# Performance work log

Hardware: AMD Instinct MI355X
Metric: run time of the kernel (lower is better)

Reference implementation:

```python
import jax, jax.numpy as jnp
import numpy as np
from jax import lax

POOL_OUT = 20  # SOCA AdaptiveAvgPool2d((20,20))
MID = 16       # out_channel // 2
BN_EPS = 1e-3


def _pool_matrix(n, out):
    # Row-stochastic matrix replicating torch AdaptiveAvgPool2d bin boundaries:
    # start = floor(i*n/out), end = ceil((i+1)*n/out)
    P = np.zeros((out, n), np.float32)
    for i in range(out):
        s = (i * n) // out
        e = -((-(i + 1) * n) // out)
        P[i, s:e] = 1.0 / (e - s)
    return jnp.asarray(P)


def setup_inputs() -> dict:
    key = jax.random.key(0)
    ks = jax.random.split(key, 5)
    B, C, H, W = 16, 256, 128, 128
    OC = 32
    x = jax.random.normal(ks[0], (B, C, H, W), dtype=jnp.float32)
    linear_w = jax.random.normal(ks[1], (C, C), dtype=jnp.float32) * (1.0 / np.sqrt(C))
    linear_b = jnp.zeros((C,), jnp.float32)
    lsa_w = jax.random.normal(ks[2], (1, 2, 7, 7), dtype=jnp.float32) * 0.1  # Conv2d(2,1,7) no bias
    conv_w = jax.random.normal(ks[3], (OC, OC, 3, 3), dtype=jnp.float32) * (1.0 / np.sqrt(OC * 9))
    conv_b = jnp.zeros((OC,), jnp.float32)
    bn_gamma = jnp.ones((OC,), jnp.float32)
    bn_beta = jnp.zeros((OC,), jnp.float32)
    return {"x": x, "linear_w": linear_w, "linear_b": linear_b, "lsa_w": lsa_w,
            "conv_w": conv_w, "conv_b": conv_b, "bn_gamma": bn_gamma, "bn_beta": bn_beta}


def _bsa_forward(x, linear_w, linear_b, lsa_w, conv_w, conv_b, bn_gamma, bn_beta):
    b, c, h, w = x.shape
    # ---- SOCA: second-order channel attention ----
    PH = _pool_matrix(h, POOL_OUT)
    PW = _pool_matrix(w, POOL_OUT)
    xp = jnp.einsum('oh,bchw,pw->bcop', PH, x, PW)          # (b,c,20,20)
    n = POOL_OUT * POOL_OUT
    v = xp.reshape(b, c, n).transpose(0, 2, 1)               # (b,400,c)
    vc = v - v.mean(axis=1, keepdims=True)
    cov = jnp.einsum('bnc,bnd->bcd', vc, vc) / (n - 1)       # (b,c,c)
    feat = cov.mean(axis=2)                                  # (b,c)
    attn = jax.nn.sigmoid(feat @ linear_w.T + linear_b)      # (b,c)
    # ---- channel scoring / top-k selection ----
    score = attn.mean(axis=0)                                # (c,)
    score_id = jnp.argsort(-score)                           # descending
    max_id = jnp.sort(score_id[:MID])                        # (MID,)
    x1 = jnp.take(x, max_id, axis=1) * (1.0 + score[max_id])[None, :, None, None]
    # ---- grouped channel mean (c divisible by MID by construction) ----
    g = c // MID
    x2 = x.reshape(b, MID, g, h, w).mean(axis=2)             # (b,MID,h,w)
    xc = jnp.concatenate([x1, x2], axis=1)                   # (b,32,h,w)
    # ---- LSA spatial attention ----
    s = jnp.concatenate([xc.mean(axis=1, keepdims=True),
                         xc.max(axis=1, keepdims=True)], axis=1)  # (b,2,h,w)
    a = lax.conv_general_dilated(s, lsa_w, (1, 1), [(3, 3), (3, 3)],
                                 dimension_numbers=('NCHW', 'OIHW', 'NCHW'))
    xa = xc * jax.nn.sigmoid(a)
    # ---- CBA: conv(3x3, stride 2) + BN(train stats) + SiLU ----
    y = lax.conv_general_dilated(xa, conv_w, (2, 2), [(1, 1), (1, 1)],
                                 dimension_numbers=('NCHW', 'OIHW', 'NCHW'))
    y = y + conv_b[None, :, None, None]
    mu = y.mean(axis=(0, 2, 3))
    var = y.var(axis=(0, 2, 3))
    yn = (y - mu[None, :, None, None]) * lax.rsqrt(var + BN_EPS)[None, :, None, None]
    yn = yn * bn_gamma[None, :, None, None] + bn_beta[None, :, None, None]
    return yn * jax.nn.sigmoid(yn)  # SiLU


def reference(x, linear_w, linear_b, lsa_w, conv_w, conv_b, bn_gamma, bn_beta):
    return _bsa_forward(x, linear_w, linear_b, lsa_w, conv_w, conv_b, bn_gamma, bn_beta)
```

## Files before the change

kernel.cpp:

```cpp
#include <hip/hip_runtime.h>
#include <math.h>

#define B_ 16
#define C_ 256
#define H_ 128
#define W_ 128
#define HW_ (H_*W_)
#define PO 20
#define NPOOL (PO*PO)
#define MID_ 16
#define OC_ 32
#define OH_ 64
#define OW_ 64
#define BN_EPS 1e-3f

#define OFF_XP     0
#define OFF_FEAT   1638400
#define OFF_SCORE  1642496
#define OFF_MAXID  1642752
#define OFF_SCALE  1642768
#define OFF_BNSUM  1642784
#define OFF_BNSQ   1642816
#define OFF_SMEAN  1642848
#define OFF_SMAX   1904992
#define OFF_SIGA   2167136
#define OFF_XC     2429280

__device__ __forceinline__ int bin_s(int p) { return (p * 128) / 20; }
__device__ __forceinline__ int bin_e(int p) { return ((p + 1) * 128 + 19) / 20; }

__global__ __launch_bounds__(256) void k_pool2(const float* __restrict__ x,
                                               float* __restrict__ xp,
                                               float* __restrict__ xc) {
  __shared__ float tmp[64 * 21];
  const int blk = blockIdx.x;
  const int b = blk >> 5, g = (blk >> 1) & 15, rh = blk & 1;
  const int tid = threadIdx.x;
  const int hl = tid >> 2, q = tid & 3;
  const int hg = rh * 64 + hl;
  const float* rowbase = x + (size_t)(b * C_) * HW_ + (size_t)hg * W_ + q * 32;

  float4 xacc[8];
#pragma unroll
  for (int j = 0; j < 8; ++j) xacc[j] = make_float4(0.f, 0.f, 0.f, 0.f);

  for (int k = 0; k < 16; ++k) {
    const int c = g * 16 + k;
    const float4* src4 = (const float4*)(rowbase + (size_t)c * HW_);
    float bin[5];
#pragma unroll
    for (int p = 0; p < 5; ++p) bin[p] = 0.f;
#pragma unroll
    for (int j = 0; j < 8; ++j) {
      float4 v = src4[j];
      xacc[j].x += v.x; xacc[j].y += v.y; xacc[j].z += v.z; xacc[j].w += v.w;
      const float c4[4] = {v.x, v.y, v.z, v.w};
#pragma unroll
      for (int kk = 0; kk < 4; ++kk) {
        const int cc = 4 * j + kk;
#pragma unroll
        for (int p = 0; p < 5; ++p) {
          const int S = (p * 32) / 5;
          const int E = ((p + 1) * 32 + 4) / 5;
          if (cc >= S && cc < E) bin[p] += c4[kk];
        }
      }
    }
#pragma unroll
    for (int p = 0; p < 5; ++p) {
      const int S = (p * 32) / 5, E = ((p + 1) * 32 + 4) / 5;
      tmp[hl * 21 + q * 5 + p] = bin[p] / (float)(E - S);
    }
    __syncthreads();
    if (tid < 200) {
      const int ol = tid / 20, p = tid % 20;
      const int o = rh * 10 + ol;
      const int rs = bin_s(o), re = bin_e(o);
      float s = 0.f;
      for (int r = rs; r < re; ++r) s += tmp[(r - rh * 64) * 21 + p];
      xp[(size_t)(b * C_ + c) * NPOOL + o * PO + p] = s / (float)(re - rs);
    }
    __syncthreads();
  }
  float4* dst = (float4*)(xc + (size_t)(b * OC_ + MID_ + g) * HW_ + (size_t)hg * W_ + q * 32);
#pragma unroll
  for (int j = 0; j < 8; ++j) {
    float4 v = xacc[j];
    v.x *= 0.0625f; v.y *= 0.0625f; v.z *= 0.0625f; v.w *= 0.0625f;
    dst[j] = v;
  }
}

__global__ __launch_bounds__(256) void k_feat(const float* __restrict__ xp,
                                              float* __restrict__ feat) {
  const int b = blockIdx.x;
  const float* base = xp + (size_t)b * C_ * NPOOL;
  const int tid = threadIdx.x;
  __shared__ float sn[NPOOL];
  __shared__ float red[256];
  const float4* row4 = (const float4*)(base + tid * NPOOL);
  float rs = 0.f;
#pragma unroll 4
  for (int n = 0; n < NPOOL / 4; ++n) {
    float4 v = row4[n];
    rs += v.x + v.y + v.z + v.w;
  }
  float m = rs / (float)NPOOL;
  red[tid] = m;
  __syncthreads();
  for (int s = 128; s > 0; s >>= 1) {
    if (tid < s) red[tid] += red[tid + s];
    __syncthreads();
  }
  float totm = red[0];
  for (int n = tid; n < NPOOL; n += 256) {
    float cs = 0.f;
    for (int c = 0; c < C_; ++c) cs += base[c * NPOOL + n];
    sn[n] = cs - totm;
  }
  __syncthreads();
  float Sl = 0.f;
  for (int n = tid; n < NPOOL; n += 256) Sl += sn[n];
  red[tid] = Sl;
  __syncthreads();
  for (int s = 128; s > 0; s >>= 1) {
    if (tid < s) red[tid] += red[tid + s];
    __syncthreads();
  }
  float S = red[0];
  float acc = 0.f;
#pragma unroll 4
  for (int n4 = 0; n4 < NPOOL / 4; ++n4) {
    float4 v = row4[n4];
    acc += v.x * sn[4 * n4] + v.y * sn[4 * n4 + 1] + v.z * sn[4 * n4 + 2] + v.w * sn[4 * n4 + 3];
  }
  feat[b * C_ + tid] = (acc - m * S) / ((float)(NPOOL - 1) * (float)C_);
}

__global__ __launch_bounds__(256) void k_attn(const float* __restrict__ feat,
                                              const float* __restrict__ lw,
                                              const float* __restrict__ lb,
                                              float* __restrict__ score) {
  __shared__ float sf[B_ * 257];
  __shared__ float wc[16 * 257];
  __shared__ float zs[16 * 17];
  const int tid = threadIdx.x;
  const int j0 = blockIdx.x * 16;
  for (int i = tid; i < B_ * C_; i += 256) sf[(i >> 8) * 257 + (i & 255)] = feat[i];
  for (int i = tid; i < 16 * C_; i += 256)
    wc[(i >> 8) * 257 + (i & 255)] = lw[(size_t)(j0 + (i >> 8)) * C_ + (i & 255)];
  __syncthreads();
  const int jl = tid >> 4, bb = tid & 15;
  float z = 0.f;
#pragma unroll 8
  for (int i = 0; i < C_; ++i) z += sf[bb * 257 + i] * wc[jl * 257 + i];
  z += lb[j0 + jl];
  zs[jl * 17 + bb] = 1.0f / (1.0f + expf(-z));
  __syncthreads();
  if (tid < 16) {
    float s = 0.f;
#pragma unroll
    for (int k = 0; k < 16; ++k) s += zs[tid * 17 + k];
    score[j0 + tid] = s / (float)B_;
  }
}

__global__ __launch_bounds__(256) void k_select(const float* __restrict__ score,
                                                int* __restrict__ max_id,
                                                float* __restrict__ scale) {
  __shared__ float ss[C_];
  __shared__ int flag[C_];
  const int tid = threadIdx.x;
  ss[tid] = score[tid];
  __syncthreads();
  float my = ss[tid];
  int rank = 0;
  for (int k = 0; k < C_; ++k) {
    float v = ss[k];
    rank += (v > my || (v == my && k < tid)) ? 1 : 0;
  }
  flag[tid] = (rank < MID_) ? 1 : 0;
  __syncthreads();
  if (rank < MID_) {
    int pos = 0;
    for (int k = 0; k < tid; ++k) pos += flag[k];
    max_id[pos] = tid;
    scale[pos] = 1.0f + my;
  }
}

__global__ __launch_bounds__(128) void k_build(const float* __restrict__ x,
                                               const int* __restrict__ max_id,
                                               const float* __restrict__ scale,
                                               float* __restrict__ xc,
                                               float* __restrict__ smean,
                                               float* __restrict__ smax) {
  __shared__ int mid_s[MID_];
  __shared__ float sc_s[MID_];
  if (threadIdx.x < MID_) {
    mid_s[threadIdx.x] = max_id[threadIdx.x];
    sc_s[threadIdx.x] = scale[threadIdx.x];
  }
  __syncthreads();
  const int P = blockIdx.x * 128 + threadIdx.x;
  const int b = P >> 12, pix4 = P & 4095;
  const float4* xb = (const float4*)x + (size_t)(b * C_) * (HW_ / 4) + pix4;
  float4* xcb = (float4*)xc + (size_t)(b * OC_) * (HW_ / 4) + pix4;
  float4 ms = make_float4(0.f, 0.f, 0.f, 0.f);
  float4 mx = make_float4(-INFINITY, -INFINITY, -INFINITY, -INFINITY);
#pragma unroll
  for (int m = 0; m < MID_; ++m) {
    float4 t = xb[(size_t)mid_s[m] * (HW_ / 4)];
    float sc = sc_s[m];
    t.x *= sc; t.y *= sc; t.z *= sc; t.w *= sc;
    xcb[(size_t)m * (HW_ / 4)] = t;
    ms.x += t.x; ms.y += t.y; ms.z += t.z; ms.w += t.w;
    mx.x = fmaxf(mx.x, t.x); mx.y = fmaxf(mx.y, t.y);
    mx.z = fmaxf(mx.z, t.z); mx.w = fmaxf(mx.w, t.w);
  }
#pragma unroll
  for (int g = 0; g < MID_; ++g) {
    float4 t = xcb[(size_t)(MID_ + g) * (HW_ / 4)];
    ms.x += t.x; ms.y += t.y; ms.z += t.z; ms.w += t.w;
    mx.x = fmaxf(mx.x, t.x); mx.y = fmaxf(mx.y, t.y);
    mx.z = fmaxf(mx.z, t.z); mx.w = fmaxf(mx.w, t.w);
  }
  ms.x *= (1.f / 32.f); ms.y *= (1.f / 32.f); ms.z *= (1.f / 32.f); ms.w *= (1.f / 32.f);
  ((float4*)smean)[P] = ms;
  ((float4*)smax)[P] = mx;
}

__global__ __launch_bounds__(256) void k_lsa(const float* __restrict__ smean,
                                             const float* __restrict__ smax,
                                             const float* __restrict__ lsa_w,
                                             float* __restrict__ siga) {
  __shared__ float w0[49], w1[49];
  if (threadIdx.x < 49) {
    w0[threadIdx.x] = lsa_w[threadIdx.x];
    w1[threadIdx.x] = lsa_w[49 + threadIdx.x];
  }
  __syncthreads();
  int idx = blockIdx.x * 256 + threadIdx.x;
  int b = idx >> 14;
  int pix = idx & (HW_ - 1);
  int h = pix >> 7, w = pix & 127;
  const float* pm = smean + (size_t)b * HW_;
  const float* px = smax + (size_t)b * HW_;
  float acc = 0.f;
  for (int kh = 0; kh < 7; ++kh) {
    int ih = h + kh - 3;
    if (ih < 0 || ih >= H_) continue;
    for (int kw = 0; kw < 7; ++kw) {
      int iw = w + kw - 3;
      if (iw < 0 || iw >= W_) continue;
      int p = ih * W_ + iw;
      acc += pm[p] * w0[kh * 7 + kw] + px[p] * w1[kh * 7 + kw];
    }
  }
  siga[idx] = 1.0f / (1.0f + __expf(-acc));
}

__global__ __launch_bounds__(256) void k_conv(const float* __restrict__ xc,
                                              const float* __restrict__ siga,
                                              const float* __restrict__ conv_w,
                                              const float* __restrict__ conv_b,
                                              float* __restrict__ out,
                                              float* __restrict__ bnsum,
                                              float* __restrict__ bnsq) {
  __shared__ __attribute__((aligned(16))) float in_lds[4 * 5 * 132];
  __shared__ float w_lds[288 * 32];
  const int tid = threadIdx.x;
  const int oc = tid & 31;
  const int g = tid >> 5;
  const int b = blockIdx.x >> 5;
  const int oh0 = (blockIdx.x & 31) * 2;
  const int ih0 = 2 * oh0 - 1;

  for (int i = tid; i < 288 * 32; i += 256) {
    int oc_ = i / 288, rem = i % 288;
    w_lds[rem * 32 + oc_] = conv_w[i];
  }

  float acc[2][8];
#pragma unroll
  for (int a = 0; a < 2; ++a)
#pragma unroll
    for (int o = 0; o < 8; ++o) acc[a][o] = 0.f;

  const float* sgb = siga + (size_t)b * HW_;

  for (int chunk = 0; chunk < 8; ++chunk) {
    __syncthreads();
    for (int i = tid; i < 4 * 5 * 132; i += 256) {
      int icl = i / 660;
      int rem = i % 660;
      int r = rem / 132, col = rem % 132;
      int ih = ih0 + r, iw = col - 1;
      float v = 0.f;
      if (ih >= 0 && ih < H_ && iw >= 0 && iw < W_) {
        int pp = ih * W_ + iw;
        v = xc[((size_t)(b * OC_) + (chunk * 4 + icl)) * HW_ + pp] * sgb[pp];
      }
      in_lds[i] = v;
    }
    __syncthreads();
#pragma unroll
    for (int icl = 0; icl < 4; ++icl) {
      const int wb = (chunk * 4 + icl) * 9 * 32 + oc;
#pragma unroll
      for (int r = 0; r < 5; ++r) {
        float f[20] __attribute__((aligned(16)));
        const float4* s4 = (const float4*)&in_lds[(icl * 5 + r) * 132 + 16 * g];
#pragma unroll
        for (int j = 0; j < 5; ++j) ((float4*)f)[j] = s4[j];
#pragma unroll
        for (int ohl = 0; ohl < 2; ++ohl) {
          const int kh = r - 2 * ohl;
          if (kh < 0 || kh > 2) continue;
          float w0 = w_lds[wb + (kh * 3 + 0) * 32];
          float w1 = w_lds[wb + (kh * 3 + 1) * 32];
          float w2 = w_lds[wb + (kh * 3 + 2) * 32];
#pragma unroll
          for (int o = 0; o < 8; ++o)
            acc[ohl][o] += f[2 * o] * w0 + f[2 * o + 1] * w1 + f[2 * o + 2] * w2;
        }
      }
    }
  }

  float bias = conv_b[oc];
  float lsum = 0.f, lsq = 0.f;
  float* outp = out + ((size_t)(b * OC_) + oc) * (OH_ * OW_) + (size_t)oh0 * OW_ + g * 8;
#pragma unroll
  for (int ohl = 0; ohl < 2; ++ohl) {
    float vout[8] __attribute__((aligned(16)));
#pragma unroll
    for (int o = 0; o < 8; ++o) {
      float v = acc[ohl][o] + bias;
      vout[o] = v;
      lsum += v;
      lsq += v * v;
    }
    *((float4*)(outp + ohl * OW_)) = *(float4*)&vout[0];
    *((float4*)(outp + ohl * OW_ + 4)) = *(float4*)&vout[4];
  }
  __syncthreads();
  in_lds[tid] = lsum;
  in_lds[256 + tid] = lsq;
  __syncthreads();
  if (tid < 32) {
    float t = 0.f, tq = 0.f;
#pragma unroll
    for (int gg = 0; gg < 8; ++gg) {
      t += in_lds[gg * 32 + tid];
      tq += in_lds[256 + gg * 32 + tid];
    }
    atomicAdd(&bnsum[tid], t);
    atomicAdd(&bnsq[tid], tq);
  }
}

__global__ __launch_bounds__(256) void k_apply(float* __restrict__ out,
                                               const float* __restrict__ sum,
                                               const float* __restrict__ sq,
                                               const float* __restrict__ gamma,
                                               const float* __restrict__ beta) {
  __shared__ float ssc[OC_], ssh[OC_];
  if (threadIdx.x < OC_) {
    int i = threadIdx.x;
    const float N = (float)(B_ * OH_ * OW_);
    float mu = sum[i] / N;
    float var = sq[i] / N - mu * mu;
    float sc = gamma[i] / sqrtf(var + BN_EPS);
    ssc[i] = sc;
    ssh[i] = beta[i] - mu * sc;
  }
  __syncthreads();
  int idx4 = blockIdx.x * 256 + threadIdx.x;
  int oc = (idx4 >> 10) & 31;
  float sc = ssc[oc], sh = ssh[oc];
  float4 v = ((float4*)out)[idx4];
  float t;
  t = v.x * sc + sh; v.x = t / (1.0f + __expf(-t));
  t = v.y * sc + sh; v.y = t / (1.0f + __expf(-t));
  t = v.z * sc + sh; v.z = t / (1.0f + __expf(-t));
  t = v.w * sc + sh; v.w = t / (1.0f + __expf(-t));
  ((float4*)out)[idx4] = v;
}

extern "C" void kernel_launch(void* const* d_in, const int* in_sizes, int n_in,
                              void* d_out, int out_size, void* d_ws, size_t ws_size,
                              hipStream_t stream) {
  const float* x      = (const float*)d_in[0];
  const float* lw     = (const float*)d_in[1];
  const float* lb     = (const float*)d_in[2];
  const float* lsa_w  = (const float*)d_in[3];
  const float* conv_w = (const float*)d_in[4];
  const float* conv_b = (const float*)d_in[5];
  const float* gamma  = (const float*)d_in[6];
  const float* beta   = (const float*)d_in[7];
  float* out = (float*)d_out;
  float* ws = (float*)d_ws;

  hipMemsetAsync(ws + OFF_BNSUM, 0, 64 * sizeof(float), stream);

  k_pool2<<<512, 256, 0, stream>>>(x, ws + OFF_XP, ws + OFF_XC);
  k_feat<<<B_, 256, 0, stream>>>(ws + OFF_XP, ws + OFF_FEAT);
  k_attn<<<16, 256, 0, stream>>>(ws + OFF_FEAT, lw, lb, ws + OFF_SCORE);
  k_select<<<1, 256, 0, stream>>>(ws + OFF_SCORE, (int*)(ws + OFF_MAXID), ws + OFF_SCALE);
  k_build<<<512, 128, 0, stream>>>(x, (const int*)(ws + OFF_MAXID), ws + OFF_SCALE,
                                   ws + OFF_XC, ws + OFF_SMEAN, ws + OFF_SMAX);
  k_lsa<<<1024, 256, 0, stream>>>(ws + OFF_SMEAN, ws + OFF_SMAX, lsa_w, ws + OFF_SIGA);
  k_conv<<<512, 256, 0, stream>>>(ws + OFF_XC, ws + OFF_SIGA, conv_w, conv_b, out,
                                  ws + OFF_BNSUM, ws + OFF_BNSQ);
  k_apply<<<2048, 256, 0, stream>>>(out, ws + OFF_BNSUM, ws + OFF_BNSQ, gamma, beta);
}
```

Before: 522.6 us.

## Fuse channel-sum into pooling, double-buffer pool LDS, split build across threads

```diff
diff --git a/kernel.cpp b/kernel.cpp
--- a/kernel.cpp
+++ b/kernel.cpp
@@ -15,24 +15,26 @@
 #define BN_EPS 1e-3f
 
 #define OFF_XP     0
-#define OFF_FEAT   1638400
-#define OFF_SCORE  1642496
-#define OFF_MAXID  1642752
-#define OFF_SCALE  1642768
-#define OFF_BNSUM  1642784
-#define OFF_BNSQ   1642816
-#define OFF_SMEAN  1642848
-#define OFF_SMAX   1904992
-#define OFF_SIGA   2167136
-#define OFF_XC     2429280
+#define OFF_SN     1638400
+#define OFF_FEAT   1644800
+#define OFF_SCORE  1648896
+#define OFF_MAXID  1649152
+#define OFF_SCALE  1649168
+#define OFF_BNSUM  1649184
+#define OFF_BNSQ   1649216
+#define OFF_SMEAN  1649248
+#define OFF_SMAX   1911392
+#define OFF_SIGA   2173536
+#define OFF_XC     2435680
 
 __device__ __forceinline__ int bin_s(int p) { return (p * 128) / 20; }
 __device__ __forceinline__ int bin_e(int p) { return ((p + 1) * 128 + 19) / 20; }
 
 __global__ __launch_bounds__(256) void k_pool2(const float* __restrict__ x,
                                                float* __restrict__ xp,
+                                               float* __restrict__ sn,
                                                float* __restrict__ xc) {
-  __shared__ float tmp[64 * 21];
+  __shared__ float tmp[2][64 * 21];
   const int blk = blockIdx.x;
   const int b = blk >> 5, g = (blk >> 1) & 15, rh = blk & 1;
   const int tid = threadIdx.x;
@@ -43,6 +45,7 @@
   float4 xacc[8];
 #pragma unroll
   for (int j = 0; j < 8; ++j) xacc[j] = make_float4(0.f, 0.f, 0.f, 0.f);
+  float snacc = 0.f;
 
   for (int k = 0; k < 16; ++k) {
     const int c = g * 16 + k;
@@ -66,10 +69,11 @@
         }
       }
     }
+    float* tb = tmp[k & 1];
 #pragma unroll
     for (int p = 0; p < 5; ++p) {
       const int S = (p * 32) / 5, E = ((p + 1) * 32 + 4) / 5;
-      tmp[hl * 21 + q * 5 + p] = bin[p] / (float)(E - S);
+      tb[hl * 21 + q * 5 + p] = bin[p] / (float)(E - S);
     }
     __syncthreads();
     if (tid < 200) {
@@ -77,11 +81,13 @@
       const int o = rh * 10 + ol;
       const int rs = bin_s(o), re = bin_e(o);
       float s = 0.f;
-      for (int r = rs; r < re; ++r) s += tmp[(r - rh * 64) * 21 + p];
-      xp[(size_t)(b * C_ + c) * NPOOL + o * PO + p] = s / (float)(re - rs);
-    }
-    __syncthreads();
-  }
+      for (int r = rs; r < re; ++r) s += tb[(r - rh * 64) * 21 + p];
+      float v = s / (float)(re - rs);
+      xp[(size_t)(b * C_ + c) * NPOOL + o * PO + p] = v;
+      snacc += v;
+    }
+  }
+  if (tid < 200) atomicAdd(&sn[b * NPOOL + rh * 200 + tid], snacc);
   float4* dst = (float4*)(xc + (size_t)(b * OC_ + MID_ + g) * HW_ + (size_t)hg * W_ + q * 32);
 #pragma unroll
   for (int j = 0; j < 8; ++j) {
@@ -92,49 +98,46 @@
 }
 
 __global__ __launch_bounds__(256) void k_feat(const float* __restrict__ xp,
+                                              const float* __restrict__ sn,
                                               float* __restrict__ feat) {
   const int b = blockIdx.x;
-  const float* base = xp + (size_t)b * C_ * NPOOL;
-  const int tid = threadIdx.x;
-  __shared__ float sn[NPOOL];
+  const int tid = threadIdx.x;
+  __shared__ float snl[NPOOL];
   __shared__ float red[256];
-  const float4* row4 = (const float4*)(base + tid * NPOOL);
+  const float4* row4 = (const float4*)(xp + (size_t)(b * C_ + tid) * NPOOL);
+  for (int i = tid; i < NPOOL; i += 256) snl[i] = sn[b * NPOOL + i];
   float rs = 0.f;
 #pragma unroll 4
   for (int n = 0; n < NPOOL / 4; ++n) {
     float4 v = row4[n];
     rs += v.x + v.y + v.z + v.w;
   }
-  float m = rs / (float)NPOOL;
-  red[tid] = m;
+  red[tid] = rs;
   __syncthreads();
   for (int s = 128; s > 0; s >>= 1) {
     if (tid < s) red[tid] += red[tid + s];
     __syncthreads();
   }
-  float totm = red[0];
-  for (int n = tid; n < NPOOL; n += 256) {
-    float cs = 0.f;
-    for (int c = 0; c < C_; ++c) cs += base[c * NPOOL + n];
-    sn[n] = cs - totm;
-  }
-  __syncthreads();
-  float Sl = 0.f;
-  for (int n = tid; n < NPOOL; n += 256) Sl += sn[n];
-  red[tid] = Sl;
+  const float totm = red[0] / (float)NPOOL;
+  __syncthreads();
+  float sl = 0.f;
+  for (int i = tid; i < NPOOL; i += 256) sl += snl[i];
+  red[tid] = sl;
   __syncthreads();
   for (int s = 128; s > 0; s >>= 1) {
     if (tid < s) red[tid] += red[tid + s];
     __syncthreads();
   }
-  float S = red[0];
-  float acc = 0.f;
+  const float S = red[0] - (float)NPOOL * totm;
+  float dot = 0.f;
 #pragma unroll 4
   for (int n4 = 0; n4 < NPOOL / 4; ++n4) {
     float4 v = row4[n4];
-    acc += v.x * sn[4 * n4] + v.y * sn[4 * n4 + 1] + v.z * sn[4 * n4 + 2] + v.w * sn[4 * n4 + 3];
-  }
-  feat[b * C_ + tid] = (acc - m * S) / ((float)(NPOOL - 1) * (float)C_);
+    dot += v.x * snl[4 * n4] + v.y * snl[4 * n4 + 1]
+         + v.z * snl[4 * n4 + 2] + v.w * snl[4 * n4 + 3];
+  }
+  const float m = rs / (float)NPOOL;
+  feat[b * C_ + tid] = (dot - totm * rs - m * S) / ((float)(NPOOL - 1) * (float)C_);
 }
 
 __global__ __launch_bounds__(256) void k_attn(const float* __restrict__ feat,
@@ -167,10 +170,12 @@
 
 __global__ __launch_bounds__(256) void k_select(const float* __restrict__ score,
                                                 int* __restrict__ max_id,
-                                                float* __restrict__ scale) {
+                                                float* __restrict__ scale,
+                                                float* __restrict__ bnzero) {
   __shared__ float ss[C_];
   __shared__ int flag[C_];
   const int tid = threadIdx.x;
+  if (tid < 64) bnzero[tid] = 0.f;
   ss[tid] = score[tid];
   __syncthreads();
   float my = ss[tid];
@@ -189,7 +194,7 @@
   }
 }
 
-__global__ __launch_bounds__(128) void k_build(const float* __restrict__ x,
+__global__ __launch_bounds__(256) void k_build(const float* __restrict__ x,
                                                const int* __restrict__ max_id,
                                                const float* __restrict__ scale,
                                                float* __restrict__ xc,
@@ -197,19 +202,23 @@
                                                float* __restrict__ smax) {
   __shared__ int mid_s[MID_];
   __shared__ float sc_s[MID_];
-  if (threadIdx.x < MID_) {
-    mid_s[threadIdx.x] = max_id[threadIdx.x];
-    sc_s[threadIdx.x] = scale[threadIdx.x];
-  }
-  __syncthreads();
-  const int P = blockIdx.x * 128 + threadIdx.x;
+  __shared__ float4 ps[128], pm[128];
+  const int tid = threadIdx.x;
+  if (tid < MID_) {
+    mid_s[tid] = max_id[tid];
+    sc_s[tid] = scale[tid];
+  }
+  __syncthreads();
+  const int p = tid & 127, s = tid >> 7;
+  const int P = blockIdx.x * 128 + p;
   const int b = P >> 12, pix4 = P & 4095;
   const float4* xb = (const float4*)x + (size_t)(b * C_) * (HW_ / 4) + pix4;
   float4* xcb = (float4*)xc + (size_t)(b * OC_) * (HW_ / 4) + pix4;
   float4 ms = make_float4(0.f, 0.f, 0.f, 0.f);
   float4 mx = make_float4(-INFINITY, -INFINITY, -INFINITY, -INFINITY);
 #pragma unroll
-  for (int m = 0; m < MID_; ++m) {
+  for (int mi = 0; mi < 8; ++mi) {
+    int m = s * 8 + mi;
     float4 t = xb[(size_t)mid_s[m] * (HW_ / 4)];
     float sc = sc_s[m];
     t.x *= sc; t.y *= sc; t.z *= sc; t.w *= sc;
@@ -219,15 +228,23 @@
     mx.z = fmaxf(mx.z, t.z); mx.w = fmaxf(mx.w, t.w);
   }
 #pragma unroll
-  for (int g = 0; g < MID_; ++g) {
-    float4 t = xcb[(size_t)(MID_ + g) * (HW_ / 4)];
+  for (int gi = 0; gi < 8; ++gi) {
+    float4 t = xcb[(size_t)(MID_ + s * 8 + gi) * (HW_ / 4)];
     ms.x += t.x; ms.y += t.y; ms.z += t.z; ms.w += t.w;
     mx.x = fmaxf(mx.x, t.x); mx.y = fmaxf(mx.y, t.y);
     mx.z = fmaxf(mx.z, t.z); mx.w = fmaxf(mx.w, t.w);
   }
-  ms.x *= (1.f / 32.f); ms.y *= (1.f / 32.f); ms.z *= (1.f / 32.f); ms.w *= (1.f / 32.f);
-  ((float4*)smean)[P] = ms;
-  ((float4*)smax)[P] = mx;
+  if (s == 1) { ps[p] = ms; pm[p] = mx; }
+  __syncthreads();
+  if (s == 0) {
+    float4 a = ps[p], m2 = pm[p];
+    ms.x = (ms.x + a.x) * (1.f / 32.f); ms.y = (ms.y + a.y) * (1.f / 32.f);
+    ms.z = (ms.z + a.z) * (1.f / 32.f); ms.w = (ms.w + a.w) * (1.f / 32.f);
+    mx.x = fmaxf(mx.x, m2.x); mx.y = fmaxf(mx.y, m2.y);
+    mx.z = fmaxf(mx.z, m2.z); mx.w = fmaxf(mx.w, m2.w);
+    ((float4*)smean)[P] = ms;
+    ((float4*)smax)[P] = mx;
+  }
 }
 
 __global__ __launch_bounds__(256) void k_lsa(const float* __restrict__ smean,
@@ -268,6 +285,7 @@
                                               float* __restrict__ bnsum,
                                               float* __restrict__ bnsq) {
   __shared__ __attribute__((aligned(16))) float in_lds[4 * 5 * 132];
+  __shared__ float sg_lds[5 * 132];
   __shared__ float w_lds[288 * 32];
   const int tid = threadIdx.x;
   const int oc = tid & 31;
@@ -280,14 +298,20 @@
     int oc_ = i / 288, rem = i % 288;
     w_lds[rem * 32 + oc_] = conv_w[i];
   }
+  const float* sgb = siga + (size_t)b * HW_;
+  for (int i = tid; i < 5 * 132; i += 256) {
+    int r = i / 132, col = i % 132;
+    int ih = ih0 + r, iw = col - 1;
+    float v = 0.f;
+    if (ih >= 0 && ih < H_ && iw >= 0 && iw < W_) v = sgb[ih * W_ + iw];
+    sg_lds[i] = v;
+  }
 
   float acc[2][8];
 #pragma unroll
   for (int a = 0; a < 2; ++a)
 #pragma unroll
     for (int o = 0; o < 8; ++o) acc[a][o] = 0.f;
-
-  const float* sgb = siga + (size_t)b * HW_;
 
   for (int chunk = 0; chunk < 8; ++chunk) {
     __syncthreads();
@@ -298,8 +322,7 @@
       int ih = ih0 + r, iw = col - 1;
       float v = 0.f;
       if (ih >= 0 && ih < H_ && iw >= 0 && iw < W_) {
-        int pp = ih * W_ + iw;
-        v = xc[((size_t)(b * OC_) + (chunk * 4 + icl)) * HW_ + pp] * sgb[pp];
+        v = xc[((size_t)(b * OC_) + (chunk * 4 + icl)) * HW_ + ih * W_ + iw] * sg_lds[rem];
       }
       in_lds[i] = v;
     }
@@ -402,13 +425,14 @@
   float* out = (float*)d_out;
   float* ws = (float*)d_ws;
 
-  hipMemsetAsync(ws + OFF_BNSUM, 0, 64 * sizeof(float), stream);
-
-  k_pool2<<<512, 256, 0, stream>>>(x, ws + OFF_XP, ws + OFF_XC);
-  k_feat<<<B_, 256, 0, stream>>>(ws + OFF_XP, ws + OFF_FEAT);
+  hipMemsetAsync(ws + OFF_SN, 0, B_ * NPOOL * sizeof(float), stream);
+
+  k_pool2<<<512, 256, 0, stream>>>(x, ws + OFF_XP, ws + OFF_SN, ws + OFF_XC);
+  k_feat<<<B_, 256, 0, stream>>>(ws + OFF_XP, ws + OFF_SN, ws + OFF_FEAT);
   k_attn<<<16, 256, 0, stream>>>(ws + OFF_FEAT, lw, lb, ws + OFF_SCORE);
-  k_select<<<1, 256, 0, stream>>>(ws + OFF_SCORE, (int*)(ws + OFF_MAXID), ws + OFF_SCALE);
-  k_build<<<512, 128, 0, stream>>>(x, (const int*)(ws + OFF_MAXID), ws + OFF_SCALE,
+  k_select<<<1, 256, 0, stream>>>(ws + OFF_SCORE, (int*)(ws + OFF_MAXID),
+                                  ws + OFF_SCALE, ws + OFF_BNSUM);
+  k_build<<<512, 256, 0, stream>>>(x, (const int*)(ws + OFF_MAXID), ws + OFF_SCALE,
                                    ws + OFF_XC, ws + OFF_SMEAN, ws + OFF_SMAX);
   k_lsa<<<1024, 256, 0, stream>>>(ws + OFF_SMEAN, ws + OFF_SMAX, lsa_w, ws + OFF_SIGA);
   k_conv<<<512, 256, 0, stream>>>(ws + OFF_XC, ws + OFF_SIGA, conv_w, conv_b, out,
```

Measured after the change: 517.6 us. No clear change (-1.0%).
